# Optimization experiments

Measured on AMD Instinct MI355X. Metric: run time of the kernel, lower is better.

Reference implementation:

```python
import jax, jax.numpy as jnp
import numpy as np

C = 512
HEADS = 4
GROUPS = 32
EPS = 1e-6


def setup_inputs() -> dict:
    key = jax.random.key(0)
    ks = jax.random.split(key, 6)
    s = 1.0 / np.sqrt(C)
    return {
        "x": jax.random.normal(ks[0], (2, C, 64, 64), dtype=jnp.float32),
        "gn_scale": jnp.ones((C,), jnp.float32),
        "gn_bias": jnp.zeros((C,), jnp.float32),
        "wq": jax.random.normal(ks[1], (C, C), jnp.float32) * s,
        "bq": jnp.zeros((C,), jnp.float32),
        "wk": jax.random.normal(ks[2], (C, C), jnp.float32) * s,
        "bk": jnp.zeros((C,), jnp.float32),
        "wv": jax.random.normal(ks[3], (C, C), jnp.float32) * s,
        "bv": jnp.zeros((C,), jnp.float32),
        "wo": jax.random.normal(ks[4], (C, C), jnp.float32) * s,
        "bo": jnp.zeros((C,), jnp.float32),
    }


def group_norm(x, scale, bias):
    # x: [b, c, h, w]; GroupNorm with 32 groups, eps 1e-6, affine
    b, c, h, w = x.shape
    xg = x.reshape(b, GROUPS, c // GROUPS, h, w)
    mean = jnp.mean(xg, axis=(2, 3, 4), keepdims=True)
    var = jnp.var(xg, axis=(2, 3, 4), keepdims=True)
    xg = (xg - mean) * jax.lax.rsqrt(var + EPS)
    x = xg.reshape(b, c, h, w)
    return x * scale[None, :, None, None] + bias[None, :, None, None]


def conv1x1(x, w, b):
    # 1x1 conv == per-pixel linear: [b,c,h,w] x [o,c] -> [b,o,h,w]
    return jnp.einsum('bchw,oc->bohw', x, w) + b[None, :, None, None]


def reference(x, gn_scale, gn_bias, wq, bq, wk, bk, wv, bv, wo, bo):
    b, c, h, w = x.shape
    hc = c // HEADS
    n = h * w

    h_ = group_norm(x, gn_scale, gn_bias)
    q = conv1x1(h_, wq, bq).reshape(b, HEADS, hc, n)
    k = conv1x1(h_, wk, bk).reshape(b, HEADS, hc, n)
    v = conv1x1(h_, wv, bv).reshape(b, HEADS, hc, n)

    # NOTE: scale uses full channel count c (repo quirk), not head_channel
    scale = jnp.asarray(c, x.dtype) ** -0.5
    scores = jnp.einsum('bhcn,bhcm->bhnm', q, k) * scale  # [b,H,N,N]
    attn = jax.nn.softmax(scores, axis=-1)
    out = jnp.einsum('bhnm,bhcm->bhcn', attn, v)  # [b,H,hc,N]

    out = out.reshape(b, c, h, w)
    return x + conv1x1(out, wo, bo)
```

## Files before the change

### kernel.cpp

```cpp
#include <hip/hip_runtime.h>

typedef float    f32x4 __attribute__((ext_vector_type(4)));
typedef short    bf16x8 __attribute__((ext_vector_type(8)));
typedef unsigned short u16;
typedef u16      u16x4 __attribute__((ext_vector_type(4)));
typedef unsigned u32;
typedef u32      u32x4 __attribute__((ext_vector_type(4)));

#define MFMA16(a, b, c) __builtin_amdgcn_mfma_f32_16x16x32_bf16((a), (b), (c), 0, 0, 0)

#define CCH 512
#define NPIX 4096
#define NHEAD 4
#define HC 128
#define NSPLIT 4
#define KVCHUNK (NPIX / NSPLIT)
#define QK_SCALE 0.04419417382415922f
#define LOG2E 1.4426950408889634f

__device__ __forceinline__ u16 f2b(float f) {
  unsigned u = __builtin_bit_cast(unsigned, f);
  u += 0x7FFFu + ((u >> 16) & 1u);
  return (u16)(u >> 16);
}
__device__ __forceinline__ float b2f(u16 b) {
  return __builtin_bit_cast(float, ((unsigned)b) << 16);
}

__device__ __forceinline__ void gl_lds16(const u16* g, u16* l) {
  __builtin_amdgcn_global_load_lds((const __attribute__((address_space(1))) void*)g,
                                   (__attribute__((address_space(3))) void*)l, 16, 0, 0);
}

__global__ void wconv_k(const float* __restrict__ w0, const float* __restrict__ w1,
                        const float* __restrict__ w2, const float* __restrict__ w3,
                        u16* __restrict__ dst) {
  int m = blockIdx.y;
  const float* src = (m == 0) ? w0 : (m == 1) ? w1 : (m == 2) ? w2 : w3;
  int i = (blockIdx.x * 256 + threadIdx.x) * 4;
  f32x4 v = *(const f32x4*)(src + i);
  u16x4 o = { f2b(v[0]), f2b(v[1]), f2b(v[2]), f2b(v[3]) };
  *(u16x4*)(dst + (size_t)m * (CCH * CCH) + i) = o;
}

__global__ void gn_stats_k(const float* __restrict__ x, float* __restrict__ pstats) {
  int blk = blockIdx.x;
  const f32x4* p = (const f32x4*)(x + (size_t)blk * 16384);
  int t = threadIdx.x, wv = t >> 6, l = t & 63;
  float s = 0.f, ss = 0.f;
  for (int i = t; i < 4096; i += 256) {
    f32x4 v = p[i];
    s  += v[0] + v[1] + v[2] + v[3];
    ss += v[0]*v[0] + v[1]*v[1] + v[2]*v[2] + v[3]*v[3];
  }
  #pragma unroll
  for (int d = 32; d; d >>= 1) { s += __shfl_down(s, d, 64); ss += __shfl_down(ss, d, 64); }
  __shared__ float red[8];
  if (l == 0) { red[wv*2] = s; red[wv*2+1] = ss; }
  __syncthreads();
  if (t == 0) {
    pstats[blk*2]   = red[0] + red[2] + red[4] + red[6];
    pstats[blk*2+1] = red[1] + red[3] + red[5] + red[7];
  }
}

__global__ void gn_norm_k(const float* __restrict__ x, const float* __restrict__ gns,
                          const float* __restrict__ gnb, const float* __restrict__ pstats,
                          u16* __restrict__ Ht) {
  int t = threadIdx.x;
  int ct = blockIdx.x * 64, nt = blockIdx.y * 64, b = blockIdx.z;
  int c0 = ct + (t & 15) * 4;
  int n0 = nt + (t >> 4) * 4;
  const float* xb = x + ((size_t)b * CCH + c0) * NPIX + n0;
  int g = b * 32 + (c0 >> 4);
  const f32x4* ps = (const f32x4*)(pstats + g * 8);
  f32x4 p0 = ps[0], p1 = ps[1];
  float s  = p0[0] + p0[2] + p1[0] + p1[2];
  float ss = p0[1] + p0[3] + p1[1] + p1[3];
  float mean = s * (1.f/65536.f);
  float var  = ss * (1.f/65536.f) - mean*mean;
  float rstd = rsqrtf(var + 1e-6f);
  f32x4 rows[4];
  #pragma unroll
  for (int j = 0; j < 4; ++j) {
    f32x4 v = *(const f32x4*)(xb + (size_t)j * NPIX);
    float a  = rstd * gns[c0 + j];
    float bb = gnb[c0 + j] - mean * a;
    rows[j] = v * a + bb;
  }
  #pragma unroll
  for (int i = 0; i < 4; ++i) {
    u16x4 o = { f2b(rows[0][i]), f2b(rows[1][i]), f2b(rows[2][i]), f2b(rows[3][i]) };
    *(u16x4*)(Ht + ((size_t)b * NPIX + n0 + i) * CCH + c0) = o;
  }
}

template<int MODE>
__global__ __launch_bounds__(256) void gemm_nt(const u16* __restrict__ A,
                                               const u16* __restrict__ B,
                                               const float* __restrict__ bias,
                                               const float* __restrict__ bias2,
                                               u16* __restrict__ outb,
                                               u16* __restrict__ outb2,
                                               float* __restrict__ outf,
                                               const float* __restrict__ resid,
                                               float alpha) {
  __shared__ __align__(16) u16 As[128 * 32];
  __shared__ __align__(16) u16 Bs[128 * 32];
  const int t = threadIdx.x, l = t & 63, wv = t >> 6;
  const int l16 = l & 15, lq = l >> 4;
  const int mt = blockIdx.x * 128, nt = blockIdx.y * 128, z = blockIdx.z;
  const u16* Ap = A + (size_t)mt * CCH;
  const u16* Bp = (MODE == 3) ? (B + (size_t)nt * CCH)
                              : (B + ((size_t)z * NPIX + nt) * CCH);
  const int wm = (wv >> 1) * 64, wn = (wv & 1) * 64;
  f32x4 acc[4][4] = {};
  for (int k0 = 0; k0 < CCH; k0 += 32) {
    __syncthreads();
    #pragma unroll
    for (int j = 0; j < 2; ++j) {
      int idx = t + j * 256;
      int row = idx >> 2, kc = (idx & 3) * 8;
      gl_lds16(Ap + (size_t)row * CCH + k0 + kc, As + idx * 8);
      gl_lds16(Bp + (size_t)row * CCH + k0 + kc, Bs + idx * 8);
    }
    __syncthreads();
    bf16x8 af[4], bfr[4];
    #pragma unroll
    for (int i = 0; i < 4; ++i) {
      af[i]  = *(const bf16x8*)(As + (wm + i * 16 + l16) * 32 + lq * 8);
      bfr[i] = *(const bf16x8*)(Bs + (wn + i * 16 + l16) * 32 + lq * 8);
    }
    #pragma unroll
    for (int mi = 0; mi < 4; ++mi)
      #pragma unroll
      for (int ni = 0; ni < 4; ++ni)
        acc[mi][ni] = MFMA16(af[mi], bfr[ni], acc[mi][ni]);
  }
  #pragma unroll
  for (int mi = 0; mi < 4; ++mi)
    #pragma unroll
    for (int ni = 0; ni < 4; ++ni)
      #pragma unroll
      for (int r = 0; r < 4; ++r) {
        int grow = mt + wm + mi * 16 + lq * 4 + r;
        int gcol = nt + wn + ni * 16 + l16;
        float v = acc[mi][ni][r];
        if (MODE == 1) {
          outb[((size_t)z * CCH + grow) * NPIX + gcol] = f2b(v + bias[grow]);
        } else if (MODE == 2) {
          size_t off = ((size_t)z * CCH + grow) * NPIX + gcol;
          outf[off] = v + bias[grow] + resid[off];
        } else {
          if (gcol < 512)
            outb[(size_t)grow * CCH + gcol] = f2b((v + bias[gcol]) * alpha);
          else
            outb2[(size_t)grow * CCH + (gcol - 512)] = f2b(v + bias2[gcol - 512]);
        }
      }
}

__global__ __launch_bounds__(512, 2) void flash_k(const u16* __restrict__ Qt,
                                                  const u16* __restrict__ Kt,
                                                  const u16* __restrict__ Vc,
                                                  u16* __restrict__ sl0, u16* __restrict__ sl1,
                                                  u16* __restrict__ sl2, u16* __restrict__ sl3,
                                                  float* __restrict__ mlp) {
  __shared__ __align__(16) char lds[65536];
  const int t = threadIdx.x, wv = t >> 6, l = t & 63;
  const int l16 = l & 15, lq = l >> 4;
  const int orig = blockIdx.x;
  const int gid = (orig & 7) * 64 + (orig >> 3);
  const int qx = gid & 15, grp = gid >> 4;
  const int hd = grp & 3, b = (grp >> 2) & 1, s = grp >> 3;
  const int qt0 = qx * 256 + wv * 32;

  const u16* Q = Qt + ((size_t)b * NPIX + qt0) * CCH + hd * HC;
  const u16* Kbase = Kt + (size_t)b * NPIX * CCH + hd * HC;
  const u16* Vbase = Vc + (size_t)b * CCH * NPIX + (size_t)hd * HC * NPIX;
  u16* slab = (s == 0) ? sl0 : (s == 1) ? sl1 : (s == 2) ? sl2 : sl3;
  u16* Ob = slab + ((size_t)(b * NHEAD + hd) * NPIX + qt0) * HC;
  size_t mlR0 = (size_t)s * 32768 + (size_t)(b * NHEAD + hd) * NPIX + qt0;

  bf16x8 qf[2][4];
  #pragma unroll
  for (int mi = 0; mi < 2; ++mi)
    #pragma unroll
    for (int kk = 0; kk < 4; ++kk)
      qf[mi][kk] = *(const bf16x8*)(Q + (size_t)(mi * 16 + l16) * CCH + kk * 32 + lq * 8);

  const int m_beg = s * KVCHUNK;
  const int sw = (l16 & 7) << 4;
  const int vb2 = (lq & 1) * 32 + (lq >> 1) * 16;

  int kbase[4], vbase[2];
  #pragma unroll
  for (int kk = 0; kk < 4; ++kk) kbase[kk] = l16 * 256 + ((kk * 64 + lq * 16) ^ sw);
  #pragma unroll
  for (int ks = 0; ks < 2; ++ks) vbase[ks] = 32768 + l16 * 128 + ((ks * 64 + vb2) ^ sw);

  u32 kgo[2], vgo[2];
  #pragma unroll
  for (int j = 0; j < 2; ++j) {
    int g = j * 512 + t;
    { int row = g >> 4, src = ((g & 15) << 4) ^ ((row & 7) << 4);
      kgo[j] = (u32)row * CCH + (src >> 1); }
    { int row = g >> 3, src = ((g & 7) << 4) ^ ((row & 7) << 4);
      vgo[j] = (u32)row * NPIX + (src >> 1); }
  }

  const short one_bf = (short)0x3F80;
  const bf16x8 vones = { one_bf, one_bf, one_bf, one_bf, one_bf, one_bf, one_bf, one_bf };

  f32x4 oacc[2][8] = {};
  f32x4 osum[2] = {};

  {
    const u16* kg = Kbase + (size_t)m_beg * CCH;
    const u16* vg = Vbase + m_beg;
    #pragma unroll
    for (int j = 0; j < 2; ++j) {
      gl_lds16(kg + kgo[j], (u16*)lds + (j * 512 + t) * 8);
      gl_lds16(vg + vgo[j], (u16*)(lds + 32768) + (j * 512 + t) * 8);
    }
  }
  asm volatile("s_waitcnt vmcnt(0)" ::: "memory");
  __syncthreads();

  const int NT = KVCHUNK / 64;

#define FLASH_BODY(CUR, M0, DOSTAGE)                                                   \
  {                                                                                    \
    if (DOSTAGE) {                                                                     \
      const u16* kg = Kbase + (size_t)((M0) + 64) * CCH;                               \
      const u16* vg = Vbase + ((M0) + 64);                                             \
      _Pragma("unroll")                                                                \
      for (int j = 0; j < 2; ++j) {                                                    \
        gl_lds16(kg + kgo[j], (u16*)(lds + ((CUR) ^ 1) * 16384) + (j * 512 + t) * 8);  \
        gl_lds16(vg + vgo[j], (u16*)(lds + 32768 + ((CUR) ^ 1) * 16384) + (j * 512 + t) * 8); \
      }                                                                                \
    }                                                                                  \
    f32x4 S[2][4] = {};                                                                \
    __builtin_amdgcn_s_setprio(1);                                                     \
    _Pragma("unroll")                                                                  \
    for (int kk = 0; kk < 4; ++kk)                                                     \
      _Pragma("unroll")                                                                \
      for (int mm = 0; mm < 4; ++mm) {                                                 \
        bf16x8 kf = *(const bf16x8*)(lds + kbase[kk] + mm * 4096 + (CUR) * 16384);     \
        S[0][mm] = MFMA16(kf, qf[0][kk], S[0][mm]);                                    \
        S[1][mm] = MFMA16(kf, qf[1][kk], S[1][mm]);                                    \
      }                                                                                \
    __builtin_amdgcn_s_setprio(0);                                                     \
    u32 pk[2][4][2];                                                                   \
    _Pragma("unroll")                                                                  \
    for (int mi = 0; mi < 2; ++mi) {                                                   \
      _Pragma("unroll")                                                                \
      for (int mm = 0; mm < 4; ++mm) {                                                 \
        f32x4 p;                                                                       \
        _Pragma("unroll")                                                              \
        for (int r = 0; r < 4; ++r) p[r] = exp2f(S[mi][mm][r]);                        \
        asm("v_cvt_pk_bf16_f32 %0, %1, %2" : "=v"(pk[mi][mm][0]) : "v"(p[0]), "v"(p[1])); \
        asm("v_cvt_pk_bf16_f32 %0, %1, %2" : "=v"(pk[mi][mm][1]) : "v"(p[2]), "v"(p[3])); \
      }                                                                                \
    }                                                                                  \
    bf16x8 pa[2][2];                                                                   \
    _Pragma("unroll")                                                                  \
    for (int mi = 0; mi < 2; ++mi)                                                     \
      _Pragma("unroll")                                                                \
      for (int ks = 0; ks < 2; ++ks) {                                                 \
        u32 a0 = pk[mi][2 * ks][0], a1 = pk[mi][2 * ks][1];                            \
        u32 b0 = pk[mi][2 * ks + 1][0], b1 = pk[mi][2 * ks + 1][1];                    \
        asm("v_permlane16_swap_b32 %0, %1" : "+v"(a0), "+v"(b0));                      \
        asm("v_permlane16_swap_b32 %0, %1" : "+v"(a1), "+v"(b1));                      \
        u32x4 w = { a0, a1, b0, b1 };                                                  \
        pa[mi][ks] = __builtin_bit_cast(bf16x8, w);                                    \
      }                                                                                \
    __builtin_amdgcn_s_setprio(1);                                                     \
    _Pragma("unroll")                                                                  \
    for (int ks = 0; ks < 2; ++ks) {                                                   \
      osum[0] = MFMA16(pa[0][ks], vones, osum[0]);                                     \
      osum[1] = MFMA16(pa[1][ks], vones, osum[1]);                                     \
      _Pragma("unroll")                                                                \
      for (int cc = 0; cc < 8; ++cc) {                                                 \
        bf16x8 vf = *(const bf16x8*)(lds + vbase[ks] + cc * 2048 + (CUR) * 16384);     \
        oacc[0][cc] = MFMA16(pa[0][ks], vf, oacc[0][cc]);                              \
        oacc[1][cc] = MFMA16(pa[1][ks], vf, oacc[1][cc]);                              \
      }                                                                                \
    }                                                                                  \
    __builtin_amdgcn_s_setprio(0);                                                     \
    asm volatile("s_waitcnt vmcnt(0)" ::: "memory");                                   \
    __syncthreads();                                                                   \
  }

  for (int it = 0; it < NT; it += 2) {
    FLASH_BODY(0, m_beg + it * 64, true)
    FLASH_BODY(1, m_beg + it * 64 + 64, (it + 2 < NT))
  }
#undef FLASH_BODY

  #pragma unroll
  for (int mi = 0; mi < 2; ++mi)
    #pragma unroll
    for (int cc = 0; cc < 8; ++cc)
      #pragma unroll
      for (int r = 0; r < 4; ++r)
        Ob[(size_t)(mi * 16 + lq * 4 + r) * HC + cc * 16 + l16] = f2b(oacc[mi][cc][r]);
  if (l16 == 0) {
    #pragma unroll
    for (int mi = 0; mi < 2; ++mi)
      #pragma unroll
      for (int r = 0; r < 4; ++r)
        mlp[mlR0 + mi * 16 + lq * 4 + r] = osum[mi][r];
  }
}

__global__ void merge_k(const u16* __restrict__ s0, const u16* __restrict__ s1,
                        const u16* __restrict__ s2, const u16* __restrict__ s3,
                        const float* __restrict__ ml, u16* __restrict__ Ot) {
  int t = threadIdx.x;
  int R = blockIdx.x * 32 + (t >> 3);
  int ch = (t & 7) * 16;
  float L = ml[R] + ml[32768 + R] + ml[65536 + R] + ml[98304 + R];
  float inv = 1.f / L;
  float acc[16] = {};
  const u16* sp[4] = { s0, s1, s2, s3 };
  #pragma unroll
  for (int s = 0; s < 4; ++s) {
    const bf16x8* p = (const bf16x8*)(sp[s] + (size_t)R * HC + ch);
    #pragma unroll
    for (int j = 0; j < 2; ++j) {
      bf16x8 v = p[j];
      #pragma unroll
      for (int e = 0; e < 8; ++e) acc[j * 8 + e] += b2f((u16)v[e]);
    }
  }
  int b = R >> 14, h = (R >> 12) & 3, q = R & 4095;
  u16* o = Ot + ((size_t)((b << 12) + q) * CCH) + h * HC + ch;
  #pragma unroll
  for (int j = 0; j < 4; ++j) {
    u16x4 o4 = { f2b(acc[j*4] * inv), f2b(acc[j*4+1] * inv),
                 f2b(acc[j*4+2] * inv), f2b(acc[j*4+3] * inv) };
    *(u16x4*)(o + j * 4) = o4;
  }
}

extern "C" void kernel_launch(void* const* d_in, const int* in_sizes, int n_in,
                              void* d_out, int out_size, void* d_ws, size_t ws_size,
                              hipStream_t stream) {
  const float* x   = (const float*)d_in[0];
  const float* gns = (const float*)d_in[1];
  const float* gnb = (const float*)d_in[2];
  const float* wq  = (const float*)d_in[3];
  const float* bq  = (const float*)d_in[4];
  const float* wk  = (const float*)d_in[5];
  const float* bk  = (const float*)d_in[6];
  const float* wv  = (const float*)d_in[7];
  const float* bv  = (const float*)d_in[8];
  const float* wo  = (const float*)d_in[9];
  const float* bo  = (const float*)d_in[10];
  float* out = (float*)d_out;
  char* ws = (char*)d_ws;

  u16*   wb    = (u16*)ws;
  u16*   Ht    = (u16*)(ws + (size_t)( 2u << 20));
  u16*   Qt    = (u16*)(ws + (size_t)(10u << 20));
  u16*   Kt    = (u16*)(ws + (size_t)(18u << 20));
  u16*   Vc    = (u16*)(ws + (size_t)(26u << 20));
  u16*   Ot    = (u16*)(ws + (size_t)(34u << 20));
  float* mlb   = (float*)(ws + (size_t)(42u << 20));
  float* stats = (float*)(ws + (size_t)(43u << 20));
  u16*   sl3   = (u16*)(ws + (size_t)(44u << 20));
  u16*   sl0   = Ht;
  u16*   sl1   = (u16*)d_out;
  u16*   sl2   = (u16*)((char*)d_out + (size_t)(8u << 20));

  wconv_k   <<<dim3(256, 4, 1), 256, 0, stream>>>(wq, wk, wv, wo, wb);
  gn_stats_k<<<dim3(256, 1, 1), 256, 0, stream>>>(x, stats);
  gn_norm_k <<<dim3(8, 64, 2),  256, 0, stream>>>(x, gns, gnb, stats, Ht);
  gemm_nt<3><<<dim3(64, 8, 1),  256, 0, stream>>>(Ht, wb, bq, bk, Qt, Kt, nullptr, nullptr,
                                                  QK_SCALE * LOG2E);
  gemm_nt<1><<<dim3(4, 32, 2),  256, 0, stream>>>(wb + 2u * 262144u, Ht, bv, nullptr, Vc, nullptr,
                                                  nullptr, nullptr, 1.0f);
  flash_k   <<<dim3(512, 1, 1), 512, 0, stream>>>(Qt, Kt, Vc, sl0, sl1, sl2, sl3, mlb);
  merge_k   <<<dim3(1024, 1, 1),256, 0, stream>>>(sl0, sl1, sl2, sl3, mlb, Ot);
  gemm_nt<2><<<dim3(4, 32, 2),  256, 0, stream>>>(wb + 3u * 262144u, Ot, bo, nullptr, nullptr,
                                                  nullptr, out, x, 1.0f);
}
```

Measured before the change: 162.6 us.

## Read V fragments directly from global memory and halve flash block size

The flash attention kernel stops staging V tiles in LDS and instead has each lane load its V fragments straight from global memory through per-channel pointers that advance each tile. Blocks shrink from 512 to 256 threads with half the LDS, and twice as many blocks are launched. The goal is to cut LDS traffic and footprint so more blocks fit per CU. The cost is uncoalesced, latency-exposed global loads of V inside the MFMA loop, which now rely on cache hits and are no longer prefetched.

After: 449.5 us. 2.77x slower.

```diff
diff --git a/kernel.cpp b/kernel.cpp
--- a/kernel.cpp
+++ b/kernel.cpp
@@ -160,20 +160,20 @@
       }
 }
 
-__global__ __launch_bounds__(512, 2) void flash_k(const u16* __restrict__ Qt,
+__global__ __launch_bounds__(256, 4) void flash_k(const u16* __restrict__ Qt,
                                                   const u16* __restrict__ Kt,
                                                   const u16* __restrict__ Vc,
                                                   u16* __restrict__ sl0, u16* __restrict__ sl1,
                                                   u16* __restrict__ sl2, u16* __restrict__ sl3,
                                                   float* __restrict__ mlp) {
-  __shared__ __align__(16) char lds[65536];
+  __shared__ __align__(16) char lds[32768];
   const int t = threadIdx.x, wv = t >> 6, l = t & 63;
   const int l16 = l & 15, lq = l >> 4;
   const int orig = blockIdx.x;
-  const int gid = (orig & 7) * 64 + (orig >> 3);
-  const int qx = gid & 15, grp = gid >> 4;
+  const int gid = (orig & 7) * 128 + (orig >> 3);
+  const int qx = gid & 31, grp = gid >> 5;
   const int hd = grp & 3, b = (grp >> 2) & 1, s = grp >> 3;
-  const int qt0 = qx * 256 + wv * 32;
+  const int qt0 = qx * 128 + wv * 32;
 
   const u16* Q = Qt + ((size_t)b * NPIX + qt0) * CCH + hd * HC;
   const u16* Kbase = Kt + (size_t)b * NPIX * CCH + hd * HC;
@@ -191,23 +191,23 @@
 
   const int m_beg = s * KVCHUNK;
   const int sw = (l16 & 7) << 4;
-  const int vb2 = (lq & 1) * 32 + (lq >> 1) * 16;
-
-  int kbase[4], vbase[2];
+
+  int kbase[4];
   #pragma unroll
   for (int kk = 0; kk < 4; ++kk) kbase[kk] = l16 * 256 + ((kk * 64 + lq * 16) ^ sw);
-  #pragma unroll
-  for (int ks = 0; ks < 2; ++ks) vbase[ks] = 32768 + l16 * 128 + ((ks * 64 + vb2) ^ sw);
-
-  u32 kgo[2], vgo[2];
-  #pragma unroll
-  for (int j = 0; j < 2; ++j) {
-    int g = j * 512 + t;
-    { int row = g >> 4, src = ((g & 15) << 4) ^ ((row & 7) << 4);
-      kgo[j] = (u32)row * CCH + (src >> 1); }
-    { int row = g >> 3, src = ((g & 7) << 4) ^ ((row & 7) << 4);
-      vgo[j] = (u32)row * NPIX + (src >> 1); }
-  }
+
+  u32 kgo[4];
+  #pragma unroll
+  for (int j = 0; j < 4; ++j) {
+    int g = j * 256 + t;
+    int row = g >> 4, src = ((g & 15) << 4) ^ ((row & 7) << 4);
+    kgo[j] = (u32)row * CCH + (src >> 1);
+  }
+
+  const u16* vp[8];
+  #pragma unroll
+  for (int cc = 0; cc < 8; ++cc)
+    vp[cc] = Vbase + (size_t)(cc * 16 + l16) * NPIX + m_beg + (lq & 1) * 16 + (lq >> 1) * 8;
 
   const short one_bf = (short)0x3F80;
   const bf16x8 vones = { one_bf, one_bf, one_bf, one_bf, one_bf, one_bf, one_bf, one_bf };
@@ -217,12 +217,8 @@
 
   {
     const u16* kg = Kbase + (size_t)m_beg * CCH;
-    const u16* vg = Vbase + m_beg;
-    #pragma unroll
-    for (int j = 0; j < 2; ++j) {
-      gl_lds16(kg + kgo[j], (u16*)lds + (j * 512 + t) * 8);
-      gl_lds16(vg + vgo[j], (u16*)(lds + 32768) + (j * 512 + t) * 8);
-    }
+    #pragma unroll
+    for (int j = 0; j < 4; ++j) gl_lds16(kg + kgo[j], (u16*)lds + (j * 256 + t) * 8);
   }
   asm volatile("s_waitcnt vmcnt(0)" ::: "memory");
   __syncthreads();
@@ -233,12 +229,9 @@
   {                                                                                    \
     if (DOSTAGE) {                                                                     \
       const u16* kg = Kbase + (size_t)((M0) + 64) * CCH;                               \
-      const u16* vg = Vbase + ((M0) + 64);                                             \
-      _Pragma("unroll")                                                                \
-      for (int j = 0; j < 2; ++j) {                                                    \
-        gl_lds16(kg + kgo[j], (u16*)(lds + ((CUR) ^ 1) * 16384) + (j * 512 + t) * 8);  \
-        gl_lds16(vg + vgo[j], (u16*)(lds + 32768 + ((CUR) ^ 1) * 16384) + (j * 512 + t) * 8); \
-      }                                                                                \
+      _Pragma("unroll")                                                                \
+      for (int j = 0; j < 4; ++j)                                                      \
+        gl_lds16(kg + kgo[j], (u16*)(lds + ((CUR) ^ 1) * 16384) + (j * 256 + t) * 8);  \
     }                                                                                  \
     f32x4 S[2][4] = {};                                                                \
     __builtin_amdgcn_s_setprio(1);                                                     \
@@ -282,12 +275,14 @@
       osum[1] = MFMA16(pa[1][ks], vones, osum[1]);                                     \
       _Pragma("unroll")                                                                \
       for (int cc = 0; cc < 8; ++cc) {                                                 \
-        bf16x8 vf = *(const bf16x8*)(lds + vbase[ks] + cc * 2048 + (CUR) * 16384);     \
+        bf16x8 vf = *(const bf16x8*)(vp[cc] + ks * 32);                                \
         oacc[0][cc] = MFMA16(pa[0][ks], vf, oacc[0][cc]);                              \
         oacc[1][cc] = MFMA16(pa[1][ks], vf, oacc[1][cc]);                              \
       }                                                                                \
     }                                                                                  \
     __builtin_amdgcn_s_setprio(0);                                                     \
+    _Pragma("unroll")                                                                  \
+    for (int cc = 0; cc < 8; ++cc) vp[cc] += 64;                                       \
     asm volatile("s_waitcnt vmcnt(0)" ::: "memory");                                   \
     __syncthreads();                                                                   \
   }
@@ -381,7 +376,7 @@
                                                   QK_SCALE * LOG2E);
   gemm_nt<1><<<dim3(4, 32, 2),  256, 0, stream>>>(wb + 2u * 262144u, Ht, bv, nullptr, Vc, nullptr,
                                                   nullptr, nullptr, 1.0f);
-  flash_k   <<<dim3(512, 1, 1), 512, 0, stream>>>(Qt, Kt, Vc, sl0, sl1, sl2, sl3, mlb);
+  flash_k   <<<dim3(1024, 1, 1), 256, 0, stream>>>(Qt, Kt, Vc, sl0, sl1, sl2, sl3, mlb);
   merge_k   <<<dim3(1024, 1, 1),256, 0, stream>>>(sl0, sl1, sl2, sl3, mlb, Ot);
   gemm_nt<2><<<dim3(4, 32, 2),  256, 0, stream>>>(wb + 3u * 262144u, Ot, bo, nullptr, nullptr,
                                                   nullptr, out, x, 1.0f);
```
